# Kernel optimization log

Measured on AMD Instinct MI355X. Metric: run time of the kernel, lower is better.

Reference implementation:

```python
import jax, jax.numpy as jnp
import numpy as np

NE, NU, E = 200000, 100000, 1000000
F_IN, H, OUT = 64, 128, 2
GRID_SIZE, K = 5, 3  # efficient-kan defaults: grid_size=5, spline_order=3
NB = GRID_SIZE + K    # number of b-spline bases per input feature = 8


def make_grid(in_features):
    h = 2.0 / GRID_SIZE  # grid_range [-1, 1]
    g = jnp.arange(-K, GRID_SIZE + K + 1, dtype=jnp.float32) * h - 1.0  # [GRID_SIZE+2K+1]
    return jnp.tile(g[None, :], (in_features, 1))  # [in, 12]


def b_splines(x, grid):
    # x: [N, in], grid: [in, G]; Cox-de Boor recursion -> [N, in, G-K-1]
    x = x[..., None]
    bases = ((x >= grid[:, :-1]) & (x < grid[:, 1:])).astype(x.dtype)
    for j in range(1, K + 1):
        bases = ((x - grid[:, :-(j + 1)]) / (grid[:, j:-1] - grid[:, :-(j + 1)])) * bases[..., :-1] \
              + ((grid[:, j + 1:] - x) / (grid[:, j + 1:] - grid[:, 1:-j])) * bases[..., 1:]
    return bases


def kan_linear(x, base_w, spline_w, scaler, grid):
    base = jax.nn.silu(x) @ base_w.T                       # [N, out]
    sw = spline_w * scaler[..., None]                      # [out, in, NB]
    spline = jnp.einsum('nik,oik->no', b_splines(x, grid), sw)
    return base + spline


def sage_conv(x_src, x_dst, ei, w_n, b_n, w_r):
    # PyG SAGEConv: lin_l(mean_j x_j) + lin_r(x_i); bias only on lin_l
    src, dst = ei[0], ei[1]
    msg = jnp.take(x_src, src, axis=0)                                  # [E, H] gather
    s = jax.ops.segment_sum(msg, dst, num_segments=x_dst.shape[0])      # scatter-sum
    cnt = jax.ops.segment_sum(jnp.ones(src.shape, x_src.dtype), dst, num_segments=x_dst.shape[0])
    mean = s / jnp.maximum(cnt, 1.0)[:, None]
    return mean @ w_n.T + b_n + x_dst @ w_r.T


def setup_inputs():
    key = jax.random.key(0)
    ks = jax.random.split(key, 40)
    inp = {}
    inp['x_email'] = jax.random.normal(ks[0], (NE, F_IN), jnp.float32)
    inp['ei_ue'] = jnp.stack([jax.random.randint(ks[1], (E,), 0, NU),
                              jax.random.randint(ks[2], (E,), 0, NE)])
    inp['ei_eu'] = jnp.stack([jax.random.randint(ks[3], (E,), 0, NE),
                              jax.random.randint(ks[4], (E,), 0, NU)])
    inp['w_email'] = jax.random.normal(ks[5], (H, F_IN), jnp.float32) * 0.05
    inp['b_email'] = jnp.zeros((H,), jnp.float32)
    inp['emb_user'] = jax.random.normal(ks[6], (NU, H), jnp.float32) * 0.05
    i = 7
    for name in ['l1_ue', 'l1_eu', 'l2_ue', 'l2_eu']:
        inp['w_' + name + '_n'] = jax.random.normal(ks[i], (H, H), jnp.float32) * 0.05; i += 1
        inp['b_' + name] = jnp.zeros((H,), jnp.float32)
        inp['w_' + name + '_r'] = jax.random.normal(ks[i], (H, H), jnp.float32) * 0.05; i += 1
    inp['kan1_base'] = jax.random.normal(ks[i], (64, H), jnp.float32) * 0.05; i += 1
    inp['kan1_spline'] = jax.random.normal(ks[i], (64, H, NB), jnp.float32) * 0.05; i += 1
    inp['kan1_scaler'] = 1.0 + jax.random.normal(ks[i], (64, H), jnp.float32) * 0.05; i += 1
    inp['grid1'] = make_grid(H)
    inp['kan2_base'] = jax.random.normal(ks[i], (OUT, 64), jnp.float32) * 0.05; i += 1
    inp['kan2_spline'] = jax.random.normal(ks[i], (OUT, 64, NB), jnp.float32) * 0.05; i += 1
    inp['kan2_scaler'] = 1.0 + jax.random.normal(ks[i], (OUT, 64), jnp.float32) * 0.05; i += 1
    inp['grid2'] = make_grid(64)
    return inp


def reference(x_email, ei_ue, ei_eu, w_email, b_email, emb_user,
              w_l1_ue_n, b_l1_ue, w_l1_ue_r, w_l1_eu_n, b_l1_eu, w_l1_eu_r,
              w_l2_ue_n, b_l2_ue, w_l2_ue_r, w_l2_eu_n, b_l2_eu, w_l2_eu_r,
              kan1_base, kan1_spline, kan1_scaler, grid1,
              kan2_base, kan2_spline, kan2_scaler, grid2):
    xe = x_email @ w_email.T + b_email      # email_lin
    xu = emb_user                            # embedding(arange(NU)) == full table
    # hetero SAGE layer 1 (to_hetero aggr='sum'; one inbound edge type per dst)
    e1 = jax.nn.relu(sage_conv(xu, xe, ei_ue, w_l1_ue_n, b_l1_ue, w_l1_ue_r))
    u1 = jax.nn.relu(sage_conv(xe, xu, ei_eu, w_l1_eu_n, b_l1_eu, w_l1_eu_r))
    # dropout(p=0.5) is identity in eval mode
    # layer 2: only the email output feeds the KAN head (user-dst conv2 output is unused)
    e2 = jax.nn.relu(sage_conv(u1, e1, ei_ue, w_l2_ue_n, b_l2_ue, w_l2_ue_r))
    h = kan_linear(e2, kan1_base, kan1_spline, kan1_scaler, grid1)
    out = kan_linear(h, kan2_base, kan2_spline, kan2_scaler, grid2)
    return out
```

## Files before the change

### kernel.cpp

```cpp
#include <hip/hip_runtime.h>
#include <hip/hip_bf16.h>

typedef __attribute__((ext_vector_type(8))) short short8;
typedef __attribute__((ext_vector_type(4))) float f32x4;

static constexpr int kNE  = 200000;
static constexpr int kNU  = 100000;
static constexpr int kE   = 1000000;

static constexpr long long SZ_NEH = (long long)kNE * 128;
static constexpr long long SZ_NUH = (long long)kNU * 128;
static constexpr long long O_B0   = 64;
static constexpr long long O_B1   = O_B0 + SZ_NEH;
static constexpr long long O_B2   = O_B1 + SZ_NEH;
static constexpr long long O_W    = O_B2 + SZ_NUH;
static constexpr long long O_BEM  = O_W;
static constexpr long long O_BL1  = O_BEM + 128;
static constexpr long long O_BEN  = O_BL1 + 128;
static constexpr long long O_BL2  = O_BEN + 128;
static constexpr long long O_GRID1= O_BL2 + 128;
static constexpr long long O_BASE2= O_GRID1 + 1536;
static constexpr long long O_GRID2= O_BASE2 + 128;
static constexpr long long O_SW2  = O_GRID2 + 768;
static constexpr long long I_CNT_UE = O_SW2 + 1024;
static constexpr long long I_CNT_EU = I_CNT_UE + kNE;
static constexpr long long I_RO_UE  = I_CNT_EU + kNU;
static constexpr long long I_RO_EU  = I_RO_UE + kNE;
static constexpr long long I_CUR_UE = I_RO_EU + kNU;
static constexpr long long I_CUR_EU = I_CUR_UE + kNE;
static constexpr long long I_SRT_UE = I_CUR_EU + kNU;
static constexpr long long I_SRT_EU = I_SRT_UE + kE;
static constexpr long long I_BSUM_UE= I_SRT_EU + kE;
static constexpr long long I_BOFF_UE= I_BSUM_UE + 256;
static constexpr long long I_BSUM_EU= I_BOFF_UE + 256;
static constexpr long long I_BOFF_EU= I_BSUM_EU + 256;
static constexpr long long FR_BASE_I= (I_BOFF_EU + 256 + 7) & ~7LL;
static constexpr long long U_WEM   = 0;
static constexpr long long U_W1N   = U_WEM + 8192;
static constexpr long long U_W1R   = U_W1N + 16384;
static constexpr long long U_WEN   = U_W1R + 16384;
static constexpr long long U_WER   = U_WEN + 16384;
static constexpr long long U_W2N   = U_WER + 16384;
static constexpr long long U_W2R   = U_W2N + 16384;
static constexpr long long U_BASE1 = U_W2R + 16384;
static constexpr long long U_SW1H  = U_BASE1 + 8192;
static constexpr long long U_SW1L  = U_SW1H + 65536;

__device__ __forceinline__ float bf2f(unsigned short u) {
    return __uint_as_float(((unsigned)u) << 16);
}
__device__ __forceinline__ unsigned short f2bf_rne(float f) {
    unsigned u = __float_as_uint(f);
    return (unsigned short)((u + 0x7fffu + ((u >> 16) & 1u)) >> 16);
}
__device__ __forceinline__ void split2(float x, unsigned short& hi, unsigned short& lo) {
    hi = f2bf_rne(x);
    lo = f2bf_rne(x - bf2f(hi));
}
__device__ __forceinline__ float btrunc(float x) {
    return __uint_as_float(__float_as_uint(x) & 0xffff0000u);
}
__device__ __forceinline__ unsigned pack_hi2(float x0, float x1) {
    return __builtin_amdgcn_perm(__float_as_uint(x1), __float_as_uint(x0), 0x07060302u);
}
__device__ __forceinline__ void split8_trunc(const float* __restrict__ xv, short8& ah, short8& al) {
    unsigned* hp = (unsigned*)&ah;
    unsigned* lp = (unsigned*)&al;
#pragma unroll
    for (int jp = 0; jp < 4; jp++) {
        const float x0 = xv[2 * jp], x1 = xv[2 * jp + 1];
        const float l0 = x0 - btrunc(x0), l1 = x1 - btrunc(x1);
        hp[jp] = pack_hi2(x0, x1);
        lp[jp] = pack_hi2(l0, l1);
    }
}
__device__ __forceinline__ int get_isbf(const unsigned* __restrict__ g) {
    return (g[0] == 0xC00CCCCDu) ? 0 : 1;
}

__device__ __forceinline__ void pack128_one(const void* __restrict__ src, unsigned short* __restrict__ dst,
                                            int K, int t, int isbf) {
    const int lane = t & 63;
    const int nt = (t >> 6) % 8;
    const int kt = (t >> 6) / 8;
    const int n = nt * 16 + (lane & 15);
    const int k0 = kt * 32 + (lane >> 4) * 8;
    unsigned short* d = dst + (((size_t)(kt * 8 + nt) * 64 + lane) << 3);
#pragma unroll
    for (int j = 0; j < 8; j++) {
        float f = isbf ? bf2f(((const unsigned short*)src)[(size_t)n * K + k0 + j])
                       : ((const float*)src)[(size_t)n * K + k0 + j];
        d[j] = f2bf_rne(f);
    }
}

__device__ __forceinline__ void base1_one(const void* __restrict__ src, unsigned short* __restrict__ dst,
                                          int t, int isbf) {
    const int lane = t & 63, nt = (t >> 6) & 3, kt = t >> 8;
    const int n = nt * 16 + (lane & 15);
    const int k0 = kt * 32 + (lane >> 4) * 8;
    unsigned short* d = dst + (((size_t)(kt * 4 + nt) * 64 + lane) << 3);
#pragma unroll
    for (int j = 0; j < 8; j++) {
        float f = isbf ? bf2f(((const unsigned short*)src)[n * 128 + k0 + j])
                       : ((const float*)src)[n * 128 + k0 + j];
        d[j] = f2bf_rne(f);
    }
}

__device__ __forceinline__ void sw1_one(const void* __restrict__ sp, const void* __restrict__ sc,
                                        unsigned short* __restrict__ dh, unsigned short* __restrict__ dl,
                                        int t, int isbf) {
    const int lane = t & 63, nt = (t >> 6) & 3, kt = t >> 8;
    const int n = nt * 16 + (lane & 15);
    const int k0 = kt * 32 + (lane >> 4) * 8;
    const float scal = isbf ? bf2f(((const unsigned short*)sc)[n * 128 + (k0 >> 3)])
                            : ((const float*)sc)[n * 128 + (k0 >> 3)];
    const size_t base = ((size_t)(kt * 4 + nt) * 64 + lane) << 3;
#pragma unroll
    for (int j = 0; j < 8; j++) {
        float f = isbf ? bf2f(((const unsigned short*)sp)[(size_t)n * 1024 + k0 + j])
                       : ((const float*)sp)[(size_t)n * 1024 + k0 + j];
        float p = f * scal;
        unsigned short hi, lo;
        split2(p, hi, lo);
        dh[base + j] = hi;
        dl[base + j] = lo;
    }
}

struct PrepArgs {
    const void* csrc[7];  int coff[7];  int cn[7];
    const void* psrc[7];  unsigned pdst[7];  int pK[7];
    const void* sp2;  const void* sc2;
    const void* b1src;  const void* swsp;  const void* swsc;
};

__global__ __launch_bounds__(256) void prep_kernel(PrepArgs A, float* __restrict__ wsf,
                                                   int* __restrict__ wsi,
                                                   unsigned short* __restrict__ fbase,
                                                   const unsigned* __restrict__ gdet) {
    const int isbf = get_isbf(gdet);
    const int t0 = blockIdx.x * 256 + threadIdx.x;
    const int gs = gridDim.x * 256;
    for (int i = t0; i < kNE + kNU; i += gs) wsi[I_CNT_UE + i] = 0;
    for (int t = 0; t < 7; t++) {
        const int n = A.cn[t];
        const void* s = A.csrc[t];
        float* d = wsf + A.coff[t];
        for (int i = t0; i < n; i += gs)
            d[i] = isbf ? bf2f(((const unsigned short*)s)[i]) : ((const float*)s)[i];
    }
    for (int i = t0; i < 1024; i += gs) {
        float a = isbf ? bf2f(((const unsigned short*)A.sp2)[i]) : ((const float*)A.sp2)[i];
        float b = isbf ? bf2f(((const unsigned short*)A.sc2)[i >> 3]) : ((const float*)A.sc2)[i >> 3];
        wsf[O_SW2 + i] = a * b;
    }
    for (int t = 0; t < 7; t++) {
        const int K = A.pK[t];
        const int tot = (K / 32) * 8 * 64;
        unsigned short* dst = fbase + A.pdst[t];
        const void* src = A.psrc[t];
        for (int i = t0; i < tot; i += gs) pack128_one(src, dst, K, i, isbf);
    }
    for (int i = t0; i < 1024; i += gs) base1_one(A.b1src, fbase + U_BASE1, i, isbf);
    for (int i = t0; i < 8192; i += gs)
        sw1_one(A.swsp, A.swsc, fbase + U_SW1H, fbase + U_SW1L, i, isbf);
}

__global__ __launch_bounds__(256) void hist_both(const int* __restrict__ ue, const int* __restrict__ eu,
                                                 int* __restrict__ cntU, int* __restrict__ cntE) {
    int i = blockIdx.x * 256 + threadIdx.x;
    if (i < kE) atomicAdd(&cntU[ue[kE + i]], 1);
    else if (i < 2 * kE) atomicAdd(&cntE[eu[kE + (i - kE)]], 1);
}

__global__ __launch_bounds__(256) void scan1_both(const int* __restrict__ cntU, int* __restrict__ roU,
                                                  int* __restrict__ bsU, const int* __restrict__ cntE,
                                                  int* __restrict__ roE, int* __restrict__ bsE) {
    __shared__ int sc[256];
    int b = blockIdx.x;
    const int* cnt;  int* ro;  int* bsum;  int n;
    if (b < 196) { cnt = cntU; ro = roU; bsum = bsU; n = kNE; }
    else { b -= 196; cnt = cntE; ro = roE; bsum = bsE; n = kNU; }
    const int t = threadIdx.x;
    const int i0 = b * 1024 + t * 4;
    int c[4];
#pragma unroll
    for (int q = 0; q < 4; q++) c[q] = (i0 + q < n) ? cnt[i0 + q] : 0;
    int s = c[0] + c[1] + c[2] + c[3];
    sc[t] = s;
    __syncthreads();
    for (int off = 1; off < 256; off <<= 1) {
        int v = (t >= off) ? sc[t - off] : 0;
        __syncthreads();
        sc[t] += v;
        __syncthreads();
    }
    int run = sc[t] - s;
#pragma unroll
    for (int q = 0; q < 4; q++) {
        if (i0 + q < n) ro[i0 + q] = run;
        run += c[q];
    }
    if (t == 255) bsum[b] = sc[255];
}

__global__ __launch_bounds__(256) void scan2_both(const int* __restrict__ bsU, int* __restrict__ boU,
                                                  const int* __restrict__ bsE, int* __restrict__ boE) {
    __shared__ int sc[256];
    const int* bsum;  int* boff;  int nb;
    if (blockIdx.x == 0) { bsum = bsU; boff = boU; nb = 196; }
    else { bsum = bsE; boff = boE; nb = 98; }
    const int t = threadIdx.x;
    int s = (t < nb) ? bsum[t] : 0;
    sc[t] = s;
    __syncthreads();
    for (int off = 1; off < 256; off <<= 1) {
        int v = (t >= off) ? sc[t - off] : 0;
        __syncthreads();
        sc[t] += v;
        __syncthreads();
    }
    if (t < nb) boff[t] = sc[t] - s;
}

__global__ __launch_bounds__(256) void scan3_both(int* __restrict__ roU, int* __restrict__ curU,
                                                  const int* __restrict__ boU, int* __restrict__ roE,
                                                  int* __restrict__ curE, const int* __restrict__ boE) {
    const int stride = gridDim.x * blockDim.x;
    for (int i = blockIdx.x * blockDim.x + threadIdx.x; i < kNE + kNU; i += stride) {
        if (i < kNE) {
            int v = roU[i] + boU[i >> 10];
            roU[i] = v;
            curU[i] = v;
        } else {
            int j = i - kNE;
            int v = roE[j] + boE[j >> 10];
            roE[j] = v;
            curE[j] = v;
        }
    }
}

__global__ __launch_bounds__(256) void fill_both(const int* __restrict__ ue, const int* __restrict__ eu,
                                                 int* __restrict__ curU, int* __restrict__ srtU,
                                                 int* __restrict__ curE, int* __restrict__ srtE) {
    int i = blockIdx.x * 256 + threadIdx.x;
    if (i < kE) {
        int pos = atomicAdd(&curU[ue[kE + i]], 1);
        srtU[pos] = ue[i];
    } else if (i < 2 * kE) {
        int j = i - kE;
        int pos = atomicAdd(&curE[eu[kE + j]], 1);
        srtE[pos] = eu[j];
    }
}

template <int KD, bool RAW, int THREADS>
__device__ __forceinline__ void stage_tile(float (*Xs)[132], const void* __restrict__ Av, int r0, int N,
                                           int tid, int isbf) {
    constexpr int TPR = THREADS / 64;
    constexpr int per = KD / TPR;
    const int row = tid / TPR;
    const int cq = (tid % TPR) * per;
    const size_t gr = (size_t)min(r0 + row, N - 1);
    if (RAW && isbf) {
        const unsigned short* p = (const unsigned short*)Av + gr * KD + cq;
#pragma unroll
        for (int v = 0; v < per; v += 8) {
            short8 s = *(const short8*)(p + v);
#pragma unroll
            for (int j = 0; j < 8; j++) Xs[row][cq + v + j] = bf2f(((unsigned short*)&s)[j]);
        }
    } else {
        const float* p = (const float*)Av + gr * KD + cq;
#pragma unroll
        for (int v = 0; v < per; v += 4) *(float4*)&Xs[row][cq + v] = *(const float4*)(p + v);
    }
}

template <int KT, int NT>
__device__ __forceinline__ void gemm_phase(float (*Xs)[132], const unsigned short* __restrict__ Wf,
                                           f32x4* acc, int rowl, int q, int lane, int ntBase) {
#pragma unroll
    for (int kt = 0; kt < KT; kt++) {
        float xv[8];
        *(float4*)&xv[0] = *(const float4*)&Xs[rowl][kt * 32 + q * 8];
        *(float4*)&xv[4] = *(const float4*)&Xs[rowl][kt * 32 + q * 8 + 4];
        short8 ah, al;
        split8_trunc(xv, ah, al);
#pragma unroll
        for (int nt = 0; nt < NT; nt++) {
            short8 b = *(const short8*)(Wf + (((size_t)(kt * 8 + ntBase + nt) * 64 + lane) << 3));
            acc[nt] = __builtin_amdgcn_mfma_f32_16x16x32_bf16(ah, b, acc[nt], 0, 0, 0);
            acc[nt] = __builtin_amdgcn_mfma_f32_16x16x32_bf16(al, b, acc[nt], 0, 0, 0);
        }
    }
}

__global__ __launch_bounds__(256) void lin_xe(const void* __restrict__ A1,
                                              const unsigned short* __restrict__ W1f,
                                              const float* __restrict__ bias, float* __restrict__ out, int N,
                                              const unsigned* __restrict__ gdet) {
    __shared__ float Xs[64][132];
    const int tid = threadIdx.x;
    const int wave = tid >> 6, lane = tid & 63;
    const int m = lane & 15, q = lane >> 4;
    const int r0 = blockIdx.x * 64;
    const int isbf = get_isbf(gdet);
    const int rowl = wave * 16 + m;
    f32x4 acc[8] = {};

    stage_tile<64, true, 256>(Xs, A1, r0, N, tid, isbf);
    __syncthreads();
    gemm_phase<2, 8>(Xs, W1f, acc, rowl, q, lane, 0);

    float bv[8];
#pragma unroll
    for (int nt = 0; nt < 8; nt++) bv[nt] = bias[nt * 16 + m];
#pragma unroll
    for (int r = 0; r < 4; r++) {
        int grow = r0 + wave * 16 + q * 4 + r;
        if (grow < N) {
#pragma unroll
            for (int nt = 0; nt < 8; nt++)
                out[(size_t)grow * 128 + nt * 16 + m] = acc[nt][r] + bv[nt];
        }
    }
}

template <bool RAWG>
__device__ __forceinline__ float2 gload(const void* __restrict__ G, int s, int lane, int isbf) {
    if (RAWG && isbf) {
        const ushort2 v = *(const ushort2*)((const unsigned short*)G + (size_t)s * 128 + lane * 2);
        return make_float2(bf2f(v.x), bf2f(v.y));
    }
    return *(const float2*)((const float*)G + (size_t)s * 128 + lane * 2);
}

template <bool RAWG, bool RAW2>
__global__ __launch_bounds__(512, 8) void agglin_mfma(const void* __restrict__ Gsrc, const void* __restrict__ A2,
                                                   const unsigned short* __restrict__ W1f,
                                                   const unsigned short* __restrict__ W2f,
                                                   const float* __restrict__ bias, float* __restrict__ out,
                                                   const int* __restrict__ ro, const int* __restrict__ cnt,
                                                   const int* __restrict__ sorted, int N,
                                                   const unsigned* __restrict__ gdet) {
    __shared__ float Xs[64][132];
    const int tid = threadIdx.x;
    const int wave = tid >> 6, lane = tid & 63;
    const int m = lane & 15, q = lane >> 4;
    const int wg = wave >> 1;
    const int wh = wave & 1;
    const int r0 = blockIdx.x * 64;
    const int isbf = get_isbf(gdet);

    for (int rr = 0; rr < 8; rr++) {
        const int lrow = wave * 8 + rr;
        const int n = r0 + lrow;
        float ax = 0.f, ay = 0.f;
        if (n < N) {
            const int beg = ro[n];
            const int end = beg + cnt[n];
            float a1x = 0.f, a1y = 0.f, a2x = 0.f, a2y = 0.f, a3x = 0.f, a3y = 0.f;
            int p = beg;
            for (; p + 3 < end; p += 4) {
                const int s0 = sorted[p], s1 = sorted[p + 1], s2 = sorted[p + 2], s3 = sorted[p + 3];
                const float2 v0 = gload<RAWG>(Gsrc, s0, lane, isbf);
                const float2 v1 = gload<RAWG>(Gsrc, s1, lane, isbf);
                const float2 v2 = gload<RAWG>(Gsrc, s2, lane, isbf);
                const float2 v3 = gload<RAWG>(Gsrc, s3, lane, isbf);
                ax += v0.x;  ay += v0.y;
                a1x += v1.x; a1y += v1.y;
                a2x += v2.x; a2y += v2.y;
                a3x += v3.x; a3y += v3.y;
            }
            for (; p < end; p++) {
                const float2 v = gload<RAWG>(Gsrc, sorted[p], lane, isbf);
                ax += v.x;
                ay += v.y;
            }
            ax += a1x + a2x + a3x;
            ay += a1y + a2y + a3y;
            const int deg = end - beg;
            const float inv = (deg > 0) ? 1.f / (float)deg : 0.f;
            ax *= inv;
            ay *= inv;
        }
        Xs[lrow][lane * 2] = ax;
        Xs[lrow][lane * 2 + 1] = ay;
    }
    __syncthreads();

    const int rowl = wg * 16 + m;
    const int ntBase = wh * 4;
    f32x4 acc[4] = {};

    gemm_phase<4, 4>(Xs, W1f, acc, rowl, q, lane, ntBase);

    __syncthreads();
    stage_tile<128, RAW2, 512>(Xs, A2, r0, N, tid, isbf);
    __syncthreads();
    gemm_phase<4, 4>(Xs, W2f, acc, rowl, q, lane, ntBase);

    float bv[4];
#pragma unroll
    for (int nt = 0; nt < 4; nt++) bv[nt] = bias[(ntBase + nt) * 16 + m];
#pragma unroll
    for (int r = 0; r < 4; r++) {
        int grow = r0 + wg * 16 + q * 4 + r;
        if (grow < N) {
#pragma unroll
            for (int nt = 0; nt < 4; nt++) {
                float v = acc[nt][r] + bv[nt];
                out[(size_t)grow * 128 + (ntBase + nt) * 16 + m] = fmaxf(v, 0.f);
            }
        }
    }
}

__device__ __forceinline__ void bases8u(float x, float t0, float invh, float* __restrict__ b) {
    const float sp = (x - t0) * invh;
    const float fi = floorf(sp);
    const float u = sp - fi;
    const int i = (int)fi;
    const float u2 = u * u, u3 = u2 * u;
    const float v = 1.f - u;
    const float p0 = u3 * (1.f / 6.f);
    const float p1 = fmaf(-0.5f, u3, fmaf(0.5f, u2, fmaf(0.5f, u, 1.f / 6.f)));
    const float p2 = fmaf(0.5f, u3, fmaf(-1.f, u2, 2.f / 3.f));
    const float p3 = v * v * v * (1.f / 6.f);
#pragma unroll
    for (int j = 0; j < 8; j++) {
        float r = (i == j) ? p0 : 0.f;
        r = (i == j + 1) ? p1 : r;
        r = (i == j + 2) ? p2 : r;
        r = (i == j + 3) ? p3 : r;
        b[j] = r;
    }
}

__device__ __forceinline__ void bases8u_frag(float x, float t0, float invh, short8& bh, short8& bl) {
    const float sp = (x - t0) * invh;
    const float fi = floorf(sp);
    const float u = sp - fi;
    int i = (int)fi;
    i = max(-1, min(11, i));
    const float u2 = u * u, u3 = u2 * u;
    const float v = 1.f - u;
    const float p0 = u3 * (1.f / 6.f);
    const float p1 = fmaf(-0.5f, u3, fmaf(0.5f, u2, fmaf(0.5f, u, 1.f / 6.f)));
    const float p2 = fmaf(0.5f, u3, fmaf(-1.f, u2, 2.f / 3.f));
    const float p3 = v * (v * v) * (1.f / 6.f);
    const float q0 = p0 - btrunc(p0), q1 = p1 - btrunc(p1);
    const float q2 = p2 - btrunc(p2), q3 = p3 - btrunc(p3);
    const unsigned long long Ph = (((unsigned long long)pack_hi2(p1, p0)) << 32) | pack_hi2(p3, p2);
    const unsigned long long Pl = (((unsigned long long)pack_hi2(q1, q0)) << 32) | pack_hi2(q3, q2);
    const int t = 16 * i - 48;
    const unsigned sa = (unsigned)t & 63u;
    const unsigned sb = (unsigned)(-t) & 63u;
    const unsigned sc = (unsigned)(64 - t) & 63u;
    const unsigned sd = (unsigned)(t - 64) & 63u;
    const bool neg = t < 0;
    const bool ok0 = t >= -48;
    const bool lt64 = t < 64;
    const bool gt0 = t > 0;
    const bool lt128 = t < 128;
    const unsigned long long h0 = neg ? (ok0 ? (Ph >> sb) : 0ull) : (lt64 ? (Ph << sa) : 0ull);
    const unsigned long long h1 = neg ? 0ull : (lt64 ? (gt0 ? (Ph >> sc) : 0ull)
                                                     : (lt128 ? (Ph << sd) : 0ull));
    const unsigned long long g0 = neg ? (ok0 ? (Pl >> sb) : 0ull) : (lt64 ? (Pl << sa) : 0ull);
    const unsigned long long g1 = neg ? 0ull : (lt64 ? (gt0 ? (Pl >> sc) : 0ull)
                                                     : (lt128 ? (Pl << sd) : 0ull));
    unsigned long long* bhp = (unsigned long long*)&bh;
    unsigned long long* blp = (unsigned long long*)&bl;
    bhp[0] = h0; bhp[1] = h1;
    blp[0] = g0; blp[1] = g1;
}

__global__ __launch_bounds__(256) void kan1_mfma(const float* __restrict__ X,
                                                 const unsigned short* __restrict__ basef,
                                                 const unsigned short* __restrict__ swh,
                                                 const unsigned short* __restrict__ swl,
                                                 const float* __restrict__ grid, float* __restrict__ Hout) {
    __shared__ float Xs[64][128];
    const int tid = threadIdx.x;
    const int wave = tid >> 6, lane = tid & 63;
    const int m = lane & 15, q = lane >> 4;
    const int r0 = blockIdx.x * 64;

    const float t0 = grid[0];
    const float invh = 1.f / (grid[1] - grid[0]);

    {
        const int row = tid >> 2, cq = (tid & 3) * 32;
        const int sw = (row & 7) << 2;
        const float* p = &X[(size_t)(r0 + row) * 128 + cq];
#pragma unroll
        for (int v = 0; v < 8; v++) *(float4*)&Xs[row][(cq + v * 4) ^ sw] = *(const float4*)(p + v * 4);
    }
    __syncthreads();

    const int rowl = wave * 16 + m;
    const int swr = (rowl & 7) << 2;
    f32x4 acc[4] = {};

#pragma unroll
    for (int kt = 0; kt < 4; kt++) {
        float xv[8];
        *(float4*)&xv[0] = *(const float4*)&Xs[rowl][(kt * 32 + q * 8) ^ swr];
        *(float4*)&xv[4] = *(const float4*)&Xs[rowl][(kt * 32 + q * 8 + 4) ^ swr];
        float sv[8];
#pragma unroll
        for (int j = 0; j < 8; j++) {
            float x = xv[j];
            sv[j] = x / (1.f + __expf(-x));
        }
        short8 ah, al;
        split8_trunc(sv, ah, al);
#pragma unroll
        for (int nt = 0; nt < 4; nt++) {
            short8 b = *(const short8*)(basef + (((size_t)(kt * 4 + nt) * 64 + lane) << 3));
            acc[nt] = __builtin_amdgcn_mfma_f32_16x16x32_bf16(ah, b, acc[nt], 0, 0, 0);
            acc[nt] = __builtin_amdgcn_mfma_f32_16x16x32_bf16(al, b, acc[nt], 0, 0, 0);
        }
    }

    const unsigned short* __restrict__ whp = swh + ((size_t)lane << 3);
    const unsigned short* __restrict__ wlp = swl + ((size_t)lane << 3);
    short8 wAh[4], wAl[4], wBh[4], wBl[4];
#pragma unroll
    for (int nt = 0; nt < 4; nt++) {
        wAh[nt] = *(const short8*)(whp + nt * 512);
        wAl[nt] = *(const short8*)(wlp + nt * 512);
    }
    float xE = Xs[rowl][q ^ swr];
#pragma unroll 1
    for (int kt2 = 0; kt2 < 16; kt2++) {
        const int ko = 2 * kt2 + 1;
#pragma unroll
        for (int nt = 0; nt < 4; nt++) {
            wBh[nt] = *(const short8*)(whp + ko * 2048 + nt * 512);
            wBl[nt] = *(const short8*)(wlp + ko * 2048 + nt * 512);
        }
        const float xO = Xs[rowl][(ko * 4 + q) ^ swr];
        {
            short8 bh, bl;
            bases8u_frag(xE, t0, invh, bh, bl);
#pragma unroll
            for (int nt = 0; nt < 4; nt++) {
                acc[nt] = __builtin_amdgcn_mfma_f32_16x16x32_bf16(bh, wAh[nt], acc[nt], 0, 0, 0);
                acc[nt] = __builtin_amdgcn_mfma_f32_16x16x32_bf16(bl, wAh[nt], acc[nt], 0, 0, 0);
                acc[nt] = __builtin_amdgcn_mfma_f32_16x16x32_bf16(bh, wAl[nt], acc[nt], 0, 0, 0);
            }
        }
        if (kt2 < 15) {
            const int ke2 = 2 * kt2 + 2;
#pragma unroll
            for (int nt = 0; nt < 4; nt++) {
                wAh[nt] = *(const short8*)(whp + ke2 * 2048 + nt * 512);
                wAl[nt] = *(const short8*)(wlp + ke2 * 2048 + nt * 512);
            }
            xE = Xs[rowl][(ke2 * 4 + q) ^ swr];
        }
        {
            short8 bh, bl;
            bases8u_frag(xO, t0, invh, bh, bl);
#pragma unroll
            for (int nt = 0; nt < 4; nt++) {
                acc[nt] = __builtin_amdgcn_mfma_f32_16x16x32_bf16(bh, wBh[nt], acc[nt], 0, 0, 0);
                acc[nt] = __builtin_amdgcn_mfma_f32_16x16x32_bf16(bl, wBh[nt], acc[nt], 0, 0, 0);
                acc[nt] = __builtin_amdgcn_mfma_f32_16x16x32_bf16(bh, wBl[nt], acc[nt], 0, 0, 0);
            }
        }
    }

#pragma unroll
    for (int r = 0; r < 4; r++) {
        int grow = r0 + wave * 16 + q * 4 + r;
#pragma unroll
        for (int nt = 0; nt < 4; nt++) Hout[(size_t)grow * 64 + nt * 16 + m] = acc[nt][r];
    }
}

__global__ __launch_bounds__(256) void kan2_kernel(const float* __restrict__ h, const float* __restrict__ base2,
                                                   const float* __restrict__ sw2, const float* __restrict__ grid2,
                                                   void* __restrict__ out, const unsigned* __restrict__ gdet) {
    const int lane = threadIdx.x & 63;
    const int wid = (blockIdx.x * blockDim.x + threadIdx.x) >> 6;
    const int nw = (gridDim.x * blockDim.x) >> 6;
    const int k = lane;
    const float t0 = grid2[0];
    const float invh = 1.f / (grid2[1] - grid2[0]);
    const float wb0 = base2[k], wb1 = base2[64 + k];
    float ws0[8], ws1[8];
#pragma unroll
    for (int j = 0; j < 8; j++) { ws0[j] = sw2[k * 8 + j]; ws1[j] = sw2[512 + k * 8 + j]; }
    const int isbf = get_isbf(gdet);

    for (int n = wid; n < kNE; n += nw) {
        float x = h[(size_t)n * 64 + k];
        float sil = x / (1.f + __expf(-x));
        float b[8];
        bases8u(x, t0, invh, b);
        float o0 = sil * wb0, o1 = sil * wb1;
#pragma unroll
        for (int j = 0; j < 8; j++) {
            o0 = fmaf(b[j], ws0[j], o0);
            o1 = fmaf(b[j], ws1[j], o1);
        }
#pragma unroll
        for (int off = 32; off > 0; off >>= 1) {
            o0 += __shfl_down(o0, off, 64);
            o1 += __shfl_down(o1, off, 64);
        }
        if (lane == 0) {
            if (isbf) {
                __hip_bfloat16* ob = (__hip_bfloat16*)out;
                ob[(size_t)n * 2] = __float2bfloat16(o0);
                ob[(size_t)n * 2 + 1] = __float2bfloat16(o1);
            } else {
                ((float2*)out)[n] = make_float2(o0, o1);
            }
        }
    }
}

extern "C" void kernel_launch(void* const* d_in, const int* in_sizes, int n_in, void* d_out, int out_size,
                              void* d_ws, size_t ws_size, hipStream_t stream) {
    (void)in_sizes; (void)n_in; (void)out_size; (void)ws_size;
    float* wsf = (float*)d_ws;
    int* wsi = (int*)d_ws;
    unsigned short* fbase = (unsigned short*)(wsi + FR_BASE_I);
    const unsigned* gdet = (const unsigned*)d_in[21];

    PrepArgs A;
    const int csrc[7] = {4, 7, 10, 13, 21, 22, 25};
    const long long coff[7] = {O_BEM, O_BL1, O_BEN, O_BL2, O_GRID1, O_BASE2, O_GRID2};
    const int cn[7] = {128, 128, 128, 128, 1536, 128, 768};
    for (int t = 0; t < 7; t++) {
        A.csrc[t] = d_in[csrc[t]];
        A.coff[t] = (int)coff[t];
        A.cn[t] = cn[t];
    }
    const int psrc[7] = {3, 6, 8, 9, 11, 12, 14};
    const long long pdst[7] = {U_WEM, U_W1N, U_W1R, U_WEN, U_WER, U_W2N, U_W2R};
    const int pK[7] = {64, 128, 128, 128, 128, 128, 128};
    for (int t = 0; t < 7; t++) {
        A.psrc[t] = d_in[psrc[t]];
        A.pdst[t] = (unsigned)pdst[t];
        A.pK[t] = pK[t];
    }
    A.sp2 = d_in[23];
    A.sc2 = d_in[24];
    A.b1src = d_in[18];
    A.swsp = d_in[19];
    A.swsc = d_in[20];
    prep_kernel<<<512, 256, 0, stream>>>(A, wsf, wsi, fbase, gdet);

    const int* ei_ue = (const int*)d_in[1];
    const int* ei_eu = (const int*)d_in[2];

    hist_both<<<(2 * kE + 255) / 256, 256, 0, stream>>>(ei_ue, ei_eu, wsi + I_CNT_UE, wsi + I_CNT_EU);
    scan1_both<<<294, 256, 0, stream>>>(wsi + I_CNT_UE, wsi + I_RO_UE, wsi + I_BSUM_UE,
                                        wsi + I_CNT_EU, wsi + I_RO_EU, wsi + I_BSUM_EU);
    scan2_both<<<2, 256, 0, stream>>>(wsi + I_BSUM_UE, wsi + I_BOFF_UE, wsi + I_BSUM_EU, wsi + I_BOFF_EU);
    scan3_both<<<512, 256, 0, stream>>>(wsi + I_RO_UE, wsi + I_CUR_UE, wsi + I_BOFF_UE,
                                        wsi + I_RO_EU, wsi + I_CUR_EU, wsi + I_BOFF_EU);
    fill_both<<<(2 * kE + 255) / 256, 256, 0, stream>>>(ei_ue, ei_eu, wsi + I_CUR_UE, wsi + I_SRT_UE,
                                                        wsi + I_CUR_EU, wsi + I_SRT_EU);

    lin_xe<<<3125, 256, 0, stream>>>(d_in[0], fbase + U_WEM, wsf + O_BEM, wsf + O_B0, kNE, gdet);

    agglin_mfma<true, false><<<3125, 512, 0, stream>>>(
        d_in[5], wsf + O_B0, fbase + U_W1N, fbase + U_W1R, wsf + O_BL1, wsf + O_B1,
        wsi + I_RO_UE, wsi + I_CNT_UE, wsi + I_SRT_UE, kNE, gdet);

    agglin_mfma<false, true><<<1563, 512, 0, stream>>>(
        wsf + O_B0, d_in[5], fbase + U_WEN, fbase + U_WER, wsf + O_BEN, wsf + O_B2,
        wsi + I_RO_EU, wsi + I_CNT_EU, wsi + I_SRT_EU, kNU, gdet);

    agglin_mfma<false, false><<<3125, 512, 0, stream>>>(
        wsf + O_B2, wsf + O_B1, fbase + U_W2N, fbase + U_W2R, wsf + O_BL2, wsf + O_B0,
        wsi + I_RO_UE, wsi + I_CNT_UE, wsi + I_SRT_UE, kNE, gdet);

    kan1_mfma<<<3125, 256, 0, stream>>>(wsf + O_B0, fbase + U_BASE1, fbase + U_SW1H, fbase + U_SW1L,
                                        wsf + O_GRID1, wsf + O_B1);
    kan2_kernel<<<2048, 256, 0, stream>>>(wsf + O_B1, wsf + O_BASE2, wsf + O_SW2, wsf + O_GRID2, d_out, gdet);
}
```

Before: 961.0 us.

## Partition histogram and fill atomics by destination range per XCD block group

The histogram and CSR fill kernels become grid-stride loops in which each block group (blockIdx mod 8) only performs atomics for destinations in its own eighth of the node range. This is meant to keep each group's atomic traffic on a disjoint slice of the counter arrays, likely matching the round-robin block placement across XCDs and reducing cross-die contention and cache-line bouncing. In exchange, every group rereads the full edge lists, which multiplies index reads by eight, and the grid is fixed at 2048 blocks.

```diff
diff --git a/kernel.cpp b/kernel.cpp
--- a/kernel.cpp
+++ b/kernel.cpp
@@ -7,6 +7,8 @@
 static constexpr int kNE  = 200000;
 static constexpr int kNU  = 100000;
 static constexpr int kE   = 1000000;
+static constexpr int kGrpU = kNE / 8;
+static constexpr int kGrpE = kNU / 8;
 
 static constexpr long long SZ_NEH = (long long)kNE * 128;
 static constexpr long long SZ_NUH = (long long)kNU * 128;
@@ -170,9 +172,16 @@
 
 __global__ __launch_bounds__(256) void hist_both(const int* __restrict__ ue, const int* __restrict__ eu,
                                                  int* __restrict__ cntU, int* __restrict__ cntE) {
-    int i = blockIdx.x * 256 + threadIdx.x;
-    if (i < kE) atomicAdd(&cntU[ue[kE + i]], 1);
-    else if (i < 2 * kE) atomicAdd(&cntE[eu[kE + (i - kE)]], 1);
+    const int g = blockIdx.x & 7;
+    const int loU = g * kGrpU, hiU = loU + kGrpU;
+    const int loE = g * kGrpE, hiE = loE + kGrpE;
+    const int stride = (gridDim.x >> 3) * 256;
+    for (int i = (blockIdx.x >> 3) * 256 + threadIdx.x; i < kE; i += stride) {
+        const int d = ue[kE + i];
+        if (d >= loU && d < hiU) atomicAdd(&cntU[d], 1);
+        const int d2 = eu[kE + i];
+        if (d2 >= loE && d2 < hiE) atomicAdd(&cntE[d2], 1);
+    }
 }
 
 __global__ __launch_bounds__(256) void scan1_both(const int* __restrict__ cntU, int* __restrict__ roU,
@@ -246,14 +255,21 @@
 __global__ __launch_bounds__(256) void fill_both(const int* __restrict__ ue, const int* __restrict__ eu,
                                                  int* __restrict__ curU, int* __restrict__ srtU,
                                                  int* __restrict__ curE, int* __restrict__ srtE) {
-    int i = blockIdx.x * 256 + threadIdx.x;
-    if (i < kE) {
-        int pos = atomicAdd(&curU[ue[kE + i]], 1);
-        srtU[pos] = ue[i];
-    } else if (i < 2 * kE) {
-        int j = i - kE;
-        int pos = atomicAdd(&curE[eu[kE + j]], 1);
-        srtE[pos] = eu[j];
+    const int g = blockIdx.x & 7;
+    const int loU = g * kGrpU, hiU = loU + kGrpU;
+    const int loE = g * kGrpE, hiE = loE + kGrpE;
+    const int stride = (gridDim.x >> 3) * 256;
+    for (int i = (blockIdx.x >> 3) * 256 + threadIdx.x; i < kE; i += stride) {
+        const int d = ue[kE + i];
+        if (d >= loU && d < hiU) {
+            const int pos = atomicAdd(&curU[d], 1);
+            srtU[pos] = ue[i];
+        }
+        const int d2 = eu[kE + i];
+        if (d2 >= loE && d2 < hiE) {
+            const int pos = atomicAdd(&curE[d2], 1);
+            srtE[pos] = eu[i];
+        }
     }
 }
 
@@ -662,14 +678,14 @@
     const int* ei_ue = (const int*)d_in[1];
     const int* ei_eu = (const int*)d_in[2];
 
-    hist_both<<<(2 * kE + 255) / 256, 256, 0, stream>>>(ei_ue, ei_eu, wsi + I_CNT_UE, wsi + I_CNT_EU);
+    hist_both<<<2048, 256, 0, stream>>>(ei_ue, ei_eu, wsi + I_CNT_UE, wsi + I_CNT_EU);
     scan1_both<<<294, 256, 0, stream>>>(wsi + I_CNT_UE, wsi + I_RO_UE, wsi + I_BSUM_UE,
                                         wsi + I_CNT_EU, wsi + I_RO_EU, wsi + I_BSUM_EU);
     scan2_both<<<2, 256, 0, stream>>>(wsi + I_BSUM_UE, wsi + I_BOFF_UE, wsi + I_BSUM_EU, wsi + I_BOFF_EU);
     scan3_both<<<512, 256, 0, stream>>>(wsi + I_RO_UE, wsi + I_CUR_UE, wsi + I_BOFF_UE,
                                         wsi + I_RO_EU, wsi + I_CUR_EU, wsi + I_BOFF_EU);
-    fill_both<<<(2 * kE + 255) / 256, 256, 0, stream>>>(ei_ue, ei_eu, wsi + I_CUR_UE, wsi + I_SRT_UE,
-                                                        wsi + I_CUR_EU, wsi + I_SRT_EU);
+    fill_both<<<2048, 256, 0, stream>>>(ei_ue, ei_eu, wsi + I_CUR_UE, wsi + I_SRT_UE,
+                                        wsi + I_CUR_EU, wsi + I_SRT_EU);
 
     lin_xe<<<3125, 256, 0, stream>>>(d_in[0], fbase + U_WEM, wsf + O_BEM, wsf + O_B0, kNE, gdet);
 
```

After: 934.2 us. -2.8%, faster.
